# Kernel optimization log

Measured on AMD Instinct MI355X. Metric: run time of the kernel, lower is better.

The kernel has to match this reference:

```python
import jax, jax.numpy as jnp
import numpy as np

N, DIM, G, K = 100000, 512, 4, 16
GD = DIM // G
EPS = 1e-5

def _ln(x, g, b):
    mu = jnp.mean(x, axis=-1, keepdims=True)
    var = jnp.mean((x - mu) ** 2, axis=-1, keepdims=True)
    return (x - mu) / jnp.sqrt(var + EPS) * g + b

def setup_inputs() -> dict:
    key = jax.random.key(0)
    ks = jax.random.split(key, 12)
    s = 1.0 / np.sqrt(GD)
    return {
        "features": jax.random.normal(ks[0], (N, DIM), jnp.float32),
        "coords": jax.random.uniform(ks[1], (N, 3), jnp.float32),
        "neighbors": jax.random.randint(ks[2], (N, K), 0, N),
        "Wq": jax.random.normal(ks[3], (G, GD, GD), jnp.float32) * s,
        "Wk": jax.random.normal(ks[4], (G, GD, GD), jnp.float32) * s,
        "Wv": jax.random.normal(ks[5], (G, GD, GD), jnp.float32) * s,
        "Wo": jax.random.normal(ks[6], (DIM, DIM), jnp.float32) / np.sqrt(DIM),
        "bo": jnp.zeros((DIM,), jnp.float32),
        "ln1_g": jnp.ones((DIM,), jnp.float32),
        "ln1_b": jnp.zeros((DIM,), jnp.float32),
        "ln2_g": jnp.ones((DIM,), jnp.float32),
        "ln2_b": jnp.zeros((DIM,), jnp.float32),
        "W1": jax.random.normal(ks[7], (2 * DIM, DIM), jnp.float32) / np.sqrt(DIM),
        "b1": jnp.zeros((2 * DIM,), jnp.float32),
        "W2": jax.random.normal(ks[8], (DIM, 2 * DIM), jnp.float32) / np.sqrt(2 * DIM),
        "b2": jnp.zeros((DIM,), jnp.float32),
    }

def reference(features, coords, neighbors, Wq, Wk, Wv, Wo, bo, ln1_g, ln1_b, ln2_g, ln2_b, W1, b1, W2, b2):
    n = features.shape[0]
    residual = features
    x = _ln(features, ln1_g, ln1_b)
    xg = x.reshape(n, G, GD)                      # chunk along feature dim == group reshape
    # per-group Linear (no bias): y = x @ W.T with W (out,in)
    q = jnp.einsum('ngd,god->ngo', xg, Wq)
    k = jnp.einsum('ngd,god->ngo', xg, Wk)
    v = jnp.einsum('ngd,god->ngo', xg, Wv)
    nk = k[neighbors]                             # (N,K,G,GD) gather
    nv = v[neighbors]
    scale = jnp.asarray(1.0 / np.sqrt(GD), x.dtype)
    scores = jnp.einsum('ngd,nkgd->nkg', q, nk) * scale
    w = jax.nn.softmax(scores, axis=1)
    attn = jnp.einsum('nkg,nkgd->ngd', w, nv).reshape(n, DIM)
    out = attn @ Wo.T + bo + residual
    res2 = out
    y = _ln(out, ln2_g, ln2_b)
    y = jax.nn.gelu(y @ W1.T + b1, approximate=False) @ W2.T + b2
    return y + res2
```

## Files before the change

### kernel.cpp

```cpp
#include <hip/hip_runtime.h>
#include <hip/hip_bf16.h>
#include <math.h>

#define NPTS 100000
#define PAD_ROWS 100096
#define DIM 512
#define GRP 4
#define GD 128
#define K_NBR 16
#define EPS 1e-5f
#define H_LD 1028

using bf16x8 = __attribute__((ext_vector_type(8))) short;
using f32x4  = __attribute__((ext_vector_type(4))) float;
using short4v = __attribute__((ext_vector_type(4))) short;

__device__ inline float bf2f(short s) {
    unsigned u = ((unsigned)(unsigned short)s) << 16;
    union { unsigned u; float f; } c; c.u = u; return c.f;
}
__device__ inline short f2bf(float f) {
    union { float f; unsigned u; } c; c.f = f;
    unsigned u = c.u;
    unsigned r = (u + 0x7fffu + ((u >> 16) & 1u)) >> 16;
    return (short)r;
}

__device__ __forceinline__ void gload_lds16(short* lds, const short* g) {
    __builtin_amdgcn_global_load_lds(
        (const __attribute__((address_space(1))) unsigned int*)g,
        (__attribute__((address_space(3))) unsigned int*)lds, 16, 0, 0);
}

__global__ void cvt_kernel(const float* __restrict__ src, short* __restrict__ dst, int n) {
    int i = blockIdx.x * blockDim.x + threadIdx.x;
    int stride = gridDim.x * blockDim.x;
    for (; i < n; i += stride) dst[i] = f2bf(src[i]);
}

__global__ void prep_m_kernel(const float* __restrict__ wq, const float* __restrict__ wk,
                              short* __restrict__ mt) {
    int ge = blockIdx.x;
    int g = ge >> 7, e = ge & 127;
    int d = threadIdx.x;
    const float* Wq = wq + (size_t)g * GD * GD;
    const float* Wk = wk + (size_t)g * GD * GD;
    float acc = 0.0f;
    for (int o = 0; o < GD; ++o)
        acc += Wq[(size_t)o * GD + d] * Wk[(size_t)o * GD + e];
    mt[(size_t)ge * GD + d] = f2bf(acc * 0.08838834764831845f);
}

__global__ void prep_wov_kernel(const float* __restrict__ wo, const float* __restrict__ wv,
                                short* __restrict__ wov) {
    int o = blockIdx.x;
    int i = threadIdx.x;
    int g = i >> 7, i0 = i & 127;
    float acc = 0.0f;
    for (int d = 0; d < GD; ++d)
        acc += wo[(size_t)o * DIM + g * GD + d] * wv[((size_t)g * GD + d) * GD + i0];
    wov[(size_t)o * DIM + i] = f2bf(acc);
}

__global__ void ln_kernel(const float* __restrict__ in, const float* __restrict__ g,
                          const float* __restrict__ b, short* __restrict__ out) {
    int row = blockIdx.x;
    int tid = threadIdx.x;
    if (row >= NPTS) {
        short4v z; z[0] = 0; z[1] = 0; z[2] = 0; z[3] = 0;
        *(short4v*)(out + (size_t)row * DIM + tid * 4) = z;
        return;
    }
    const float4 x = *(const float4*)(in + (size_t)row * DIM + tid * 4);
    float s  = x.x + x.y + x.z + x.w;
    float sq = x.x * x.x + x.y * x.y + x.z * x.z + x.w * x.w;
    for (int m = 1; m < 64; m <<= 1) {
        s  += __shfl_xor(s, m);
        sq += __shfl_xor(sq, m);
    }
    __shared__ float ss[2], ssq[2];
    int wv = tid >> 6;
    if ((tid & 63) == 0) { ss[wv] = s; ssq[wv] = sq; }
    __syncthreads();
    s = ss[0] + ss[1]; sq = ssq[0] + ssq[1];
    float mu = s * (1.0f / DIM);
    float var = sq * (1.0f / DIM) - mu * mu;
    float rstd = rsqrtf(var + EPS);
    const float4 gg = *(const float4*)(g + tid * 4);
    const float4 bb = *(const float4*)(b + tid * 4);
    short4v o;
    o[0] = f2bf((x.x - mu) * rstd * gg.x + bb.x);
    o[1] = f2bf((x.y - mu) * rstd * gg.y + bb.y);
    o[2] = f2bf((x.z - mu) * rstd * gg.z + bb.z);
    o[3] = f2bf((x.w - mu) * rstd * gg.w + bb.w);
    *(short4v*)(out + (size_t)row * DIM + tid * 4) = o;
}

__global__ void ln_bf16_kernel(const short* __restrict__ in, const float* __restrict__ g,
                               const float* __restrict__ b, short* __restrict__ out) {
    int row = blockIdx.x;
    int tid = threadIdx.x;
    if (row >= NPTS) {
        short4v z; z[0] = 0; z[1] = 0; z[2] = 0; z[3] = 0;
        *(short4v*)(out + (size_t)row * DIM + tid * 4) = z;
        return;
    }
    short4v xi = *(const short4v*)(in + (size_t)row * DIM + tid * 4);
    float x0 = bf2f(xi[0]), x1 = bf2f(xi[1]), x2 = bf2f(xi[2]), x3 = bf2f(xi[3]);
    float s  = x0 + x1 + x2 + x3;
    float sq = x0 * x0 + x1 * x1 + x2 * x2 + x3 * x3;
    for (int m = 1; m < 64; m <<= 1) {
        s  += __shfl_xor(s, m);
        sq += __shfl_xor(sq, m);
    }
    __shared__ float ss[2], ssq[2];
    int wv = tid >> 6;
    if ((tid & 63) == 0) { ss[wv] = s; ssq[wv] = sq; }
    __syncthreads();
    s = ss[0] + ss[1]; sq = ssq[0] + ssq[1];
    float mu = s * (1.0f / DIM);
    float var = sq * (1.0f / DIM) - mu * mu;
    float rstd = rsqrtf(var + EPS);
    const float4 gg = *(const float4*)(g + tid * 4);
    const float4 bb = *(const float4*)(b + tid * 4);
    short4v o;
    o[0] = f2bf((x0 - mu) * rstd * gg.x + bb.x);
    o[1] = f2bf((x1 - mu) * rstd * gg.y + bb.y);
    o[2] = f2bf((x2 - mu) * rstd * gg.z + bb.z);
    o[3] = f2bf((x3 - mu) * rstd * gg.w + bb.w);
    *(short4v*)(out + (size_t)row * DIM + tid * 4) = o;
}

__device__ __forceinline__ void stage_tile(short* As, short* Bs,
        const short* aS, int as_, const short* bS, int bs_, int tid) {
    int ldRow = tid >> 2;
    int ldCol = (tid & 3) * 8;
    gload_lds16(As + (ldRow)      * 32 + ldCol, aS + (size_t)(ldRow)      * as_ + ldCol);
    gload_lds16(As + (ldRow + 64) * 32 + ldCol, aS + (size_t)(ldRow + 64) * as_ + ldCol);
    gload_lds16(Bs + (ldRow)      * 32 + ldCol, bS + (size_t)(ldRow)      * bs_ + ldCol);
    gload_lds16(Bs + (ldRow + 64) * 32 + ldCol, bS + (size_t)(ldRow + 64) * bs_ + ldCol);
}

__device__ __forceinline__ void compute_tile(const short* As, const short* Bs,
        int wr, int wc, int r, int ks, f32x4 (&acc)[4][4]) {
    bf16x8 a[4];
    #pragma unroll
    for (int m = 0; m < 4; ++m)
        a[m] = *(const bf16x8*)(As + (wr * 64 + m * 16 + r) * 32 + ks * 8);
    #pragma unroll
    for (int n = 0; n < 4; ++n) {
        bf16x8 b = *(const bf16x8*)(Bs + (wc * 64 + n * 16 + r) * 32 + ks * 8);
        #pragma unroll
        for (int m = 0; m < 4; ++m)
            acc[m][n] = __builtin_amdgcn_mfma_f32_16x16x32_bf16(a[m], b, acc[m][n], 0, 0, 0);
    }
}

template<int NK>
__device__ __forceinline__ void gemm_tile(
        const short* __restrict__ aBase, int as_,
        const short* __restrict__ bBase, int bs_,
        short* As0, short* Bs0, short* As1, short* Bs1, f32x4 (&acc)[4][4]) {
    int tid = threadIdx.x;
    int lane = tid & 63, wave = tid >> 6;
    int wr = wave >> 1, wc = wave & 1;
    int r = lane & 15, ks = lane >> 4;
    stage_tile(As0, Bs0, aBase, as_, bBase, bs_, tid);
    __syncthreads();
    #pragma unroll
    for (int kt = 0; kt < NK; kt += 2) {
        if (kt + 1 < NK)
            stage_tile(As1, Bs1, aBase + (kt + 1) * 32, as_, bBase + (kt + 1) * 32, bs_, tid);
        compute_tile(As0, Bs0, wr, wc, r, ks, acc);
        __syncthreads();
        if (kt + 2 < NK)
            stage_tile(As0, Bs0, aBase + (kt + 2) * 32, as_, bBase + (kt + 2) * 32, bs_, tid);
        compute_tile(As1, Bs1, wr, wc, r, ks, acc);
        __syncthreads();
    }
}

#define GEMM_LDS \
    __shared__ short As0[128 * 32], Bs0[128 * 32], As1[128 * 32], Bs1[128 * 32]

__global__ __launch_bounds__(256) void qproj_kernel(
        const short* __restrict__ x, const short* __restrict__ mt,
        short* __restrict__ qp) {
    GEMM_LDS;
    int nwg = gridDim.x;
    int bid = blockIdx.x;
    int tile = (bid & 7) * (nwg >> 3) + (bid >> 3);
    int rb = tile >> 2, g = tile & 3;
    int rowbase = rb * 128;
    int tid = threadIdx.x;
    int lane = tid & 63, wave = tid >> 6;
    int wr = wave >> 1, wc = wave & 1;
    int r = lane & 15, ks = lane >> 4;
    f32x4 acc[4][4];
    #pragma unroll
    for (int m = 0; m < 4; ++m)
        #pragma unroll
        for (int n = 0; n < 4; ++n)
            #pragma unroll
            for (int e = 0; e < 4; ++e) acc[m][n][e] = 0.0f;
    gemm_tile<4>(x + (size_t)rowbase * DIM + g * GD, DIM,
                 mt + (size_t)g * GD * GD, GD, As0, Bs0, As1, Bs1, acc);
    #pragma unroll
    for (int m = 0; m < 4; ++m)
        #pragma unroll
        for (int n = 0; n < 4; ++n)
            #pragma unroll
            for (int rr = 0; rr < 4; ++rr) {
                int orow = rowbase + wr * 64 + m * 16 + ks * 4 + rr;
                int lcol = wc * 64 + n * 16 + r;
                qp[(size_t)orow * DIM + g * GD + lcol] = f2bf(acc[m][n][rr]);
            }
}

__global__ __launch_bounds__(256) void attn_kernel(
        const short* __restrict__ qp, const short* __restrict__ x,
        const int* __restrict__ nbrs, short* __restrict__ t_out) {
    int b = blockIdx.x;
    int xcd = b & 7;
    int g = xcd >> 1;
    int quad = (b >> 3) * 2 + (xcd & 1);
    int tid = threadIdx.x;
    int wv = tid >> 6, lane = tid & 63;
    int n = quad * 4 + wv;
    int s = lane >> 4, t = lane & 15;
    int4 nbj = *(const int4*)(nbrs + (size_t)n * K_NBR + s * 4);
    int nbarr[4] = {nbj.x, nbj.y, nbj.z, nbj.w};
    size_t goff = (size_t)g * GD + t * 8;
    size_t qbase = (size_t)n * DIM + goff;
    bf16x8 qf = *(const bf16x8*)(qp + qbase);
    float qv[8];
    #pragma unroll
    for (int e = 0; e < 8; ++e) qv[e] = bf2f(qf[e]);
    bf16x8 xf[4];
    #pragma unroll
    for (int p = 0; p < 4; ++p)
        xf[p] = *(const bf16x8*)(x + (size_t)nbarr[p] * DIM + goff);
    float sc[4];
    #pragma unroll
    for (int p = 0; p < 4; ++p) {
        float dd = 0.0f;
        #pragma unroll
        for (int e = 0; e < 8; ++e) dd += qv[e] * bf2f(xf[p][e]);
        dd += __shfl_xor(dd, 1);
        dd += __shfl_xor(dd, 2);
        dd += __shfl_xor(dd, 4);
        dd += __shfl_xor(dd, 8);
        sc[p] = dd;
    }
    float mx = fmaxf(fmaxf(sc[0], sc[1]), fmaxf(sc[2], sc[3]));
    mx = fmaxf(mx, __shfl_xor(mx, 16));
    mx = fmaxf(mx, __shfl_xor(mx, 32));
    float ew[4]; float ssum = 0.0f;
    #pragma unroll
    for (int p = 0; p < 4; ++p) { ew[p] = __expf(sc[p] - mx); ssum += ew[p]; }
    ssum += __shfl_xor(ssum, 16);
    ssum += __shfl_xor(ssum, 32);
    float acc[8];
    #pragma unroll
    for (int d0 = 0; d0 < 8; ++d0) acc[d0] = 0.0f;
    #pragma unroll
    for (int p = 0; p < 4; ++p) {
        #pragma unroll
        for (int d0 = 0; d0 < 8; ++d0) acc[d0] += ew[p] * bf2f(xf[p][d0]);
    }
    #pragma unroll
    for (int d0 = 0; d0 < 8; ++d0) {
        acc[d0] += __shfl_xor(acc[d0], 16);
        acc[d0] += __shfl_xor(acc[d0], 32);
    }
    if (s == 0) {
        float inv = 1.0f / ssum;
        bf16x8 o;
        #pragma unroll
        for (int d0 = 0; d0 < 8; ++d0) o[d0] = f2bf(acc[d0] * inv);
        *(bf16x8*)(t_out + qbase) = o;
    }
}

__global__ __launch_bounds__(256) void outproj_kernel(
        const short* __restrict__ tbuf, const short* __restrict__ wov,
        const float* __restrict__ bo, const float* __restrict__ features,
        short* __restrict__ res2) {
    GEMM_LDS;
    int nwg = gridDim.x;
    int bid = blockIdx.x;
    int tile = (bid & 7) * (nwg >> 3) + (bid >> 3);
    int rb = tile >> 2, cb = tile & 3;
    int rowbase = rb * 128, colbase = cb * 128;
    int tid = threadIdx.x;
    int lane = tid & 63, wave = tid >> 6;
    int wr = wave >> 1, wc = wave & 1;
    int r = lane & 15, ks = lane >> 4;
    f32x4 acc[4][4];
    #pragma unroll
    for (int m = 0; m < 4; ++m)
        #pragma unroll
        for (int n = 0; n < 4; ++n)
            #pragma unroll
            for (int e = 0; e < 4; ++e) acc[m][n][e] = 0.0f;
    gemm_tile<16>(tbuf + (size_t)rowbase * DIM, DIM,
                  wov + (size_t)colbase * DIM, DIM, As0, Bs0, As1, Bs1, acc);
    #pragma unroll
    for (int m = 0; m < 4; ++m)
        #pragma unroll
        for (int n = 0; n < 4; ++n)
            #pragma unroll
            for (int rr = 0; rr < 4; ++rr) {
                int orow = rowbase + wr * 64 + m * 16 + ks * 4 + rr;
                int ocol = colbase + wc * 64 + n * 16 + r;
                if (orow < NPTS) {
                    float val = acc[m][n][rr] + bo[ocol] + features[(size_t)orow * DIM + ocol];
                    res2[(size_t)orow * DIM + ocol] = f2bf(val);
                }
            }
}

__global__ __launch_bounds__(512) void ffn_fused_kernel(
        const short* __restrict__ y, const short* __restrict__ w1,
        const float* __restrict__ b1, const short* __restrict__ w2,
        const float* __restrict__ b2, const short* __restrict__ res2,
        float* __restrict__ out) {
    __shared__ short hbuf[64 * H_LD];
    __shared__ short Ab[2][64 * 64];
    int tid = threadIdx.x;
    int lane = tid & 63, wave = tid >> 6;
    int r = lane & 15, ks = lane >> 4;
    int rowbase = blockIdx.x * 64;
    const short* yR = y + (size_t)rowbase * DIM;
    int srow = tid >> 3, schunk = tid & 7;

    f32x4 acc1[4][8];
    #pragma unroll
    for (int m = 0; m < 4; ++m)
        #pragma unroll
        for (int n = 0; n < 8; ++n)
            #pragma unroll
            for (int e = 0; e < 4; ++e) acc1[m][n][e] = 0.0f;
    int colbase1 = wave * 128;
    gload_lds16(Ab[0] + srow * 64 + schunk * 8,
                yR + (size_t)srow * DIM + 0 + ((schunk ^ (srow & 7)) * 8));
    __syncthreads();
    for (int kt = 0; kt < 8; ++kt) {
        if (kt + 1 < 8)
            gload_lds16(Ab[(kt + 1) & 1] + srow * 64 + schunk * 8,
                        yR + (size_t)srow * DIM + (kt + 1) * 64 + ((schunk ^ (srow & 7)) * 8));
        const short* A = Ab[kt & 1];
        #pragma unroll
        for (int ks2 = 0; ks2 < 2; ++ks2) {
            int kc8 = ((ks2 * 4 + ks) ^ (r & 7)) * 8;
            bf16x8 a[4];
            #pragma unroll
            for (int m = 0; m < 4; ++m)
                a[m] = *(const bf16x8*)(A + (m * 16 + r) * 64 + kc8);
            int kg = kt * 64 + ks2 * 32 + ks * 8;
            #pragma unroll
            for (int n = 0; n < 8; ++n) {
                bf16x8 b = *(const bf16x8*)(w1 + (size_t)(colbase1 + n * 16 + r) * DIM + kg);
                #pragma unroll
                for (int m = 0; m < 4; ++m)
                    acc1[m][n] = __builtin_amdgcn_mfma_f32_16x16x32_bf16(a[m], b, acc1[m][n], 0, 0, 0);
            }
        }
        __syncthreads();
    }
    #pragma unroll
    for (int m = 0; m < 4; ++m)
        #pragma unroll
        for (int n = 0; n < 8; ++n) {
            int hcol = colbase1 + n * 16 + r;
            float bb = b1[hcol];
            #pragma unroll
            for (int rr = 0; rr < 4; ++rr) {
                int hrow = m * 16 + ks * 4 + rr;
                float xv = acc1[m][n][rr] + bb;
                float xc = fminf(fmaxf(xv, -9.0f), 9.0f);
                float u = xc * (0.7978845608028654f + 0.0356774081f * xc * xc);
                float e2 = __expf(2.0f * u);
                float th = (e2 - 1.0f) / (e2 + 1.0f);
                hbuf[hrow * H_LD + hcol] = f2bf(0.5f * xv * (1.0f + th));
            }
        }
    __syncthreads();

    f32x4 acc2[4][4];
    #pragma unroll
    for (int m = 0; m < 4; ++m)
        #pragma unroll
        for (int n = 0; n < 4; ++n)
            #pragma unroll
            for (int e = 0; e < 4; ++e) acc2[m][n][e] = 0.0f;
    int colbase2 = wave * 64;
    for (int k2 = 0; k2 < 1024; k2 += 32) {
        bf16x8 a[4];
        #pragma unroll
        for (int m = 0; m < 4; ++m)
            a[m] = *(const bf16x8*)(hbuf + (m * 16 + r) * H_LD + k2 + ks * 8);
        #pragma unroll
        for (int n = 0; n < 4; ++n) {
            bf16x8 b = *(const bf16x8*)(w2 + (size_t)(colbase2 + n * 16 + r) * 1024 + k2 + ks * 8);
            #pragma unroll
            for (int m = 0; m < 4; ++m)
                acc2[m][n] = __builtin_amdgcn_mfma_f32_16x16x32_bf16(a[m], b, acc2[m][n], 0, 0, 0);
        }
    }
    #pragma unroll
    for (int m = 0; m < 4; ++m)
        #pragma unroll
        for (int n = 0; n < 4; ++n)
            #pragma unroll
            for (int rr = 0; rr < 4; ++rr) {
                int orow = rowbase + m * 16 + ks * 4 + rr;
                int ocol = colbase2 + n * 16 + r;
                if (orow < NPTS) {
                    size_t idx = (size_t)orow * DIM + ocol;
                    out[idx] = acc2[m][n][rr] + b2[ocol] + bf2f(res2[idx]);
                }
            }
}

extern "C" void kernel_launch(void* const* d_in, const int* in_sizes, int n_in,
                              void* d_out, int out_size, void* d_ws, size_t ws_size,
                              hipStream_t stream) {
    const float* features = (const float*)d_in[0];
    const int*   neighbors = (const int*)d_in[2];
    const float* Wq = (const float*)d_in[3];
    const float* Wk = (const float*)d_in[4];
    const float* Wv = (const float*)d_in[5];
    const float* Wo = (const float*)d_in[6];
    const float* bo = (const float*)d_in[7];
    const float* ln1_g = (const float*)d_in[8];
    const float* ln1_b = (const float*)d_in[9];
    const float* ln2_g = (const float*)d_in[10];
    const float* ln2_b = (const float*)d_in[11];
    const float* W1 = (const float*)d_in[12];
    const float* b1 = (const float*)d_in[13];
    const float* W2 = (const float*)d_in[14];
    const float* b2 = (const float*)d_in[15];
    float* out = (float*)d_out;

    size_t slotElems = (size_t)PAD_ROWS * DIM;
    short* s0 = (short*)d_ws;
    short* s1 = s0 + slotElems;
    short* s2 = s1 + slotElems;
    short* s3 = s2 + slotElems;
    short* mt_b  = s3 + slotElems;
    short* wov_b = mt_b + GRP * GD * GD;
    short* w1_b  = wov_b + DIM * DIM;
    short* w2_b  = w1_b + 2 * DIM * DIM;

    cvt_kernel<<<256, 256, 0, stream>>>(W1, w1_b, 2 * DIM * DIM);
    cvt_kernel<<<256, 256, 0, stream>>>(W2, w2_b, 2 * DIM * DIM);
    prep_m_kernel<<<GRP * GD, GD, 0, stream>>>(Wq, Wk, mt_b);
    prep_wov_kernel<<<DIM, DIM, 0, stream>>>(Wo, Wv, wov_b);

    ln_kernel<<<PAD_ROWS, 128, 0, stream>>>(features, ln1_g, ln1_b, s0);

    qproj_kernel<<<(PAD_ROWS / 128) * 4, 256, 0, stream>>>(s0, mt_b, s1);

    attn_kernel<<<NPTS, 256, 0, stream>>>(s1, s0, neighbors, s2);

    outproj_kernel<<<(PAD_ROWS / 128) * 4, 256, 0, stream>>>(s2, wov_b, bo, features, s3);

    ln_bf16_kernel<<<PAD_ROWS, 128, 0, stream>>>(s3, ln2_g, ln2_b, s0);

    ffn_fused_kernel<<<PAD_ROWS / 64, 512, 0, stream>>>(s0, w1_b, b1, w2_b, b2, s3, out);
}
```

Before: 1.316 ms.

## Halve FFN row tile to 32 rows, swizzle hidden buffer, raise occupancy

After: 1.456 ms. 10.7% more time.

```diff
diff --git a/kernel.cpp b/kernel.cpp
--- a/kernel.cpp
+++ b/kernel.cpp
@@ -9,7 +9,6 @@
 #define GD 128
 #define K_NBR 16
 #define EPS 1e-5f
-#define H_LD 1028
 
 using bf16x8 = __attribute__((ext_vector_type(8))) short;
 using f32x4  = __attribute__((ext_vector_type(4))) float;
@@ -320,56 +319,54 @@
             }
 }
 
-__global__ __launch_bounds__(512) void ffn_fused_kernel(
+__global__ __launch_bounds__(512, 4) void ffn_fused_kernel(
         const short* __restrict__ y, const short* __restrict__ w1,
         const float* __restrict__ b1, const short* __restrict__ w2,
         const float* __restrict__ b2, const short* __restrict__ res2,
         float* __restrict__ out) {
-    __shared__ short hbuf[64 * H_LD];
-    __shared__ short Ab[2][64 * 64];
+    __shared__ short hbuf[32 * 1024];
+    __shared__ short ybuf[32 * 64];
     int tid = threadIdx.x;
     int lane = tid & 63, wave = tid >> 6;
     int r = lane & 15, ks = lane >> 4;
-    int rowbase = blockIdx.x * 64;
+    int rowbase = blockIdx.x * 32;
     const short* yR = y + (size_t)rowbase * DIM;
-    int srow = tid >> 3, schunk = tid & 7;
-
-    f32x4 acc1[4][8];
-    #pragma unroll
-    for (int m = 0; m < 4; ++m)
+
+    f32x4 acc1[2][8];
+    #pragma unroll
+    for (int m = 0; m < 2; ++m)
         #pragma unroll
         for (int n = 0; n < 8; ++n)
             #pragma unroll
             for (int e = 0; e < 4; ++e) acc1[m][n][e] = 0.0f;
     int colbase1 = wave * 128;
-    gload_lds16(Ab[0] + srow * 64 + schunk * 8,
-                yR + (size_t)srow * DIM + 0 + ((schunk ^ (srow & 7)) * 8));
-    __syncthreads();
     for (int kt = 0; kt < 8; ++kt) {
-        if (kt + 1 < 8)
-            gload_lds16(Ab[(kt + 1) & 1] + srow * 64 + schunk * 8,
-                        yR + (size_t)srow * DIM + (kt + 1) * 64 + ((schunk ^ (srow & 7)) * 8));
-        const short* A = Ab[kt & 1];
+        if (tid < 256) {
+            int srow = tid >> 3, sc = tid & 7;
+            gload_lds16(ybuf + tid * 8,
+                        yR + (size_t)srow * DIM + kt * 64 + ((sc ^ (srow & 7)) * 8));
+        }
+        __syncthreads();
         #pragma unroll
         for (int ks2 = 0; ks2 < 2; ++ks2) {
             int kc8 = ((ks2 * 4 + ks) ^ (r & 7)) * 8;
-            bf16x8 a[4];
-            #pragma unroll
-            for (int m = 0; m < 4; ++m)
-                a[m] = *(const bf16x8*)(A + (m * 16 + r) * 64 + kc8);
+            bf16x8 a[2];
+            #pragma unroll
+            for (int m = 0; m < 2; ++m)
+                a[m] = *(const bf16x8*)(ybuf + (m * 16 + r) * 64 + kc8);
             int kg = kt * 64 + ks2 * 32 + ks * 8;
             #pragma unroll
             for (int n = 0; n < 8; ++n) {
                 bf16x8 b = *(const bf16x8*)(w1 + (size_t)(colbase1 + n * 16 + r) * DIM + kg);
                 #pragma unroll
-                for (int m = 0; m < 4; ++m)
+                for (int m = 0; m < 2; ++m)
                     acc1[m][n] = __builtin_amdgcn_mfma_f32_16x16x32_bf16(a[m], b, acc1[m][n], 0, 0, 0);
             }
         }
         __syncthreads();
     }
     #pragma unroll
-    for (int m = 0; m < 4; ++m)
+    for (int m = 0; m < 2; ++m)
         #pragma unroll
         for (int n = 0; n < 8; ++n) {
             int hcol = colbase1 + n * 16 + r;
@@ -382,34 +379,39 @@
                 float u = xc * (0.7978845608028654f + 0.0356774081f * xc * xc);
                 float e2 = __expf(2.0f * u);
                 float th = (e2 - 1.0f) / (e2 + 1.0f);
-                hbuf[hrow * H_LD + hcol] = f2bf(0.5f * xv * (1.0f + th));
+                int chunk = hcol >> 3, within = hcol & 7;
+                hbuf[hrow * 1024 + ((chunk ^ (hrow & 7)) << 3) + within] =
+                    f2bf(0.5f * xv * (1.0f + th));
             }
         }
     __syncthreads();
 
-    f32x4 acc2[4][4];
-    #pragma unroll
-    for (int m = 0; m < 4; ++m)
+    f32x4 acc2[2][4];
+    #pragma unroll
+    for (int m = 0; m < 2; ++m)
         #pragma unroll
         for (int n = 0; n < 4; ++n)
             #pragma unroll
             for (int e = 0; e < 4; ++e) acc2[m][n][e] = 0.0f;
     int colbase2 = wave * 64;
     for (int k2 = 0; k2 < 1024; k2 += 32) {
-        bf16x8 a[4];
-        #pragma unroll
-        for (int m = 0; m < 4; ++m)
-            a[m] = *(const bf16x8*)(hbuf + (m * 16 + r) * H_LD + k2 + ks * 8);
+        bf16x8 a[2];
+        #pragma unroll
+        for (int m = 0; m < 2; ++m) {
+            int row = m * 16 + r;
+            int chunk = (k2 >> 3) + ks;
+            a[m] = *(const bf16x8*)(hbuf + row * 1024 + ((chunk ^ (row & 7)) << 3));
+        }
         #pragma unroll
         for (int n = 0; n < 4; ++n) {
             bf16x8 b = *(const bf16x8*)(w2 + (size_t)(colbase2 + n * 16 + r) * 1024 + k2 + ks * 8);
             #pragma unroll
-            for (int m = 0; m < 4; ++m)
+            for (int m = 0; m < 2; ++m)
                 acc2[m][n] = __builtin_amdgcn_mfma_f32_16x16x32_bf16(a[m], b, acc2[m][n], 0, 0, 0);
         }
     }
     #pragma unroll
-    for (int m = 0; m < 4; ++m)
+    for (int m = 0; m < 2; ++m)
         #pragma unroll
         for (int n = 0; n < 4; ++n)
             #pragma unroll
@@ -468,5 +470,5 @@
 
     ln_bf16_kernel<<<PAD_ROWS, 128, 0, stream>>>(s3, ln2_g, ln2_b, s0);
 
-    ffn_fused_kernel<<<PAD_ROWS / 64, 512, 0, stream>>>(s0, w1_b, b1, w2_b, b2, s3, out);
-}
+    ffn_fused_kernel<<<PAD_ROWS / 32, 512, 0, stream>>>(s0, w1_b, b1, w2_b, b2, s3, out);
+}
```
